# Kernel optimization log

Hardware: AMD Instinct MI355X
Metric: run time of the kernel (lower is better)

## Reference

```python
import jax, jax.numpy as jnp
import numpy as np

B, L, D = 4, 4096, 1024
NEG_BIG = -1e30  # finite stand-in for log(0) to keep vjp NaN-free; exp underflows to 0


def log_g(x):
    # log of g(x) = where(x>=0, x+0.5, sigmoid(x)); log-space, branch-safe
    return jnp.where(x >= 0.0, jnp.log(jax.nn.relu(x) + 0.5), -jax.nn.softplus(-x))


def setup_inputs() -> dict:
    key = jax.random.key(0)
    ks = jax.random.split(key, 4)
    std = np.sqrt(2.0 / D)  # kaiming_normal for fan_in = D
    x = jax.random.normal(ks[0], (B, L, D), dtype=jnp.float32)
    W_f = jax.random.normal(ks[1], (D, D), dtype=jnp.float32) * std
    W_i = jax.random.normal(ks[2], (D, D), dtype=jnp.float32) * std
    W_h = jax.random.normal(ks[3], (D, D), dtype=jnp.float32) * std
    b_f = jnp.zeros((D,), dtype=jnp.float32)
    b_i = jnp.zeros((D,), dtype=jnp.float32)
    b_h = jnp.zeros((D,), dtype=jnp.float32)
    return {"x": x, "W_f": W_f, "b_f": b_f, "W_i": W_i, "b_i": b_i, "W_h": W_h, "b_h": b_h}


def reference(x, W_f, b_f, W_i, b_i, W_h, b_h):
    # gate pre-activations: (B, L, D)
    f_pre = jnp.einsum('bld,ed->ble', x, W_f) + b_f
    i_pre = jnp.einsum('bld,ed->ble', x, W_i) + b_i
    h_pre = jnp.einsum('bld,ed->ble', x, W_h) + b_h

    # log-space normalized gates: log_f + log_i parametrize f/(f+i), i/(f+i)
    diff = jax.nn.softplus(-f_pre) - jax.nn.softplus(-i_pre)
    log_f = -jax.nn.softplus(diff)
    log_i = -jax.nn.softplus(-diff)
    log_tilde_h = log_g(h_pre)

    b, l, d = x.shape
    log_h0 = jnp.full((b, 1, d), NEG_BIG, dtype=x.dtype)  # log(0)
    log_values = jnp.concatenate([log_h0, log_i + log_tilde_h], axis=1)  # (B, L+1, D)

    # associative parallel scan in log space
    a_star = jnp.pad(jnp.cumsum(log_f, axis=1), ((0, 0), (1, 0), (0, 0)))  # (B, L+1, D)
    log_h = a_star + jax.lax.cumlogsumexp(log_values - a_star, axis=1)
    return jnp.exp(log_h)[:, 1:]  # (B, L, D)
```

## Files before the change

### kernel.cpp

```cpp
#include <hip/hip_runtime.h>

#define M_TOTAL 16384
#define N_DIM   1024
#define K_DIM   1024
#define L_SEQ   4096
#define B_SZ    4
#define D_DIM   1024
#define CH      64
#define NCHUNK  (L_SEQ / CH)
#define NCHAN   (B_SZ * D_DIM)

#define BM 128
#define BN 128
#define BK 64
#define NKT (K_DIM / BK)
#define TPB 512

typedef __attribute__((ext_vector_type(8))) short v8s;
typedef __attribute__((ext_vector_type(4))) float f32x4;

#define SB0()   __builtin_amdgcn_sched_barrier(0)
#define BAR()   __builtin_amdgcn_s_barrier()
#define WAITL0() do { asm volatile("s_waitcnt lgkmcnt(0)" ::: "memory"); SB0(); } while (0)
#define WAITL4() do { asm volatile("s_waitcnt lgkmcnt(4)" ::: "memory"); SB0(); } while (0)
#define WAITV0() do { asm volatile("s_waitcnt vmcnt(0)"   ::: "memory"); SB0(); } while (0)
#define AS1 __attribute__((address_space(1)))
#define AS3 __attribute__((address_space(3)))

__device__ __forceinline__ ushort f2b(float f) {
  uint u = __float_as_uint(f);
  u += 0x7FFFu + ((u >> 16) & 1u);
  return (ushort)(u >> 16);
}
__device__ __forceinline__ float b2f(ushort u) {
  return __uint_as_float(((uint)u) << 16);
}

__global__ void cast_f32_bf16(const float* __restrict__ src, ushort* __restrict__ dst, int n4) {
  int i = blockIdx.x * blockDim.x + threadIdx.x;
  if (i >= n4) return;
  float4 v = reinterpret_cast<const float4*>(src)[i];
  ushort4 o = make_ushort4(f2b(v.x), f2b(v.y), f2b(v.z), f2b(v.w));
  reinterpret_cast<ushort4*>(dst)[i] = o;
}

__device__ __forceinline__ void gates(float fp, float ip, float hp, float& a, float& v) {
  float Ef = __expf(-fp);
  float Ei = __expf(-ip);
  float r  = __builtin_amdgcn_rcpf(2.f + Ef + Ei);
  float f  = (1.f + Ei) * r;
  float i  = (1.f + Ef) * r;
  float ht = (hp >= 0.f) ? (hp + 0.5f) : __builtin_amdgcn_rcpf(1.f + __expf(-hp));
  a = f;
  v = i * ht;
}

__launch_bounds__(TPB, 2)
__global__ void gemm_fused(const ushort* __restrict__ X,
                           const ushort* __restrict__ W0, const ushort* __restrict__ W1,
                           const ushort* __restrict__ W2,
                           const float* __restrict__ bfp, const float* __restrict__ bip,
                           const float* __restrict__ bhp,
                           uint* __restrict__ Pav)
{
  __shared__ ushort lds[2][4][BM * BK];

  const int id = blockIdx.x;
  const int sw = (id & 7) * 128 + (id >> 3);
  const int n0 = (sw & 7) * BN;
  const int m0 = (sw >> 3) * BM;

  const int tid  = threadIdx.x;
  const int lane = tid & 63;
  const int w    = tid >> 6;
  const int wr   = w >> 2;
  const int wc   = w & 3;
  const int fr   = lane & 15, g = lane >> 4;

  int aoffh[4][2], boffh[2][2];
#pragma unroll
  for (int q = 0; q < 4; ++q)
#pragma unroll
    for (int ks = 0; ks < 2; ++ks) {
      int row = wr * 64 + q * 16 + fr;
      aoffh[q][ks] = row * BK + (((ks * 4 + g) ^ (row & 7)) << 3);
    }
#pragma unroll
  for (int n = 0; n < 2; ++n)
#pragma unroll
    for (int ks = 0; ks < 2; ++ks) {
      int row = wc * 32 + n * 16 + fr;
      boffh[n][ks] = row * BK + (((ks * 4 + g) ^ (row & 7)) << 3);
    }

  const int s0 = tid, s1 = 512 + tid;
  const int r0 = s0 >> 3, k0 = (s0 & 7) ^ (r0 & 7);
  const int r1 = s1 >> 3, k1 = (s1 & 7) ^ (r1 & 7);
  const int d0 = s0 * 8, d1 = s1 * 8;

  const ushort* gsrc[4][2];
  gsrc[0][0] = X  + (size_t)(m0 + r0) * K_DIM + k0 * 8;
  gsrc[0][1] = X  + (size_t)(m0 + r1) * K_DIM + k1 * 8;
  gsrc[1][0] = W0 + (size_t)(n0 + r0) * K_DIM + k0 * 8;
  gsrc[1][1] = W0 + (size_t)(n0 + r1) * K_DIM + k1 * 8;
  gsrc[2][0] = W1 + (size_t)(n0 + r0) * K_DIM + k0 * 8;
  gsrc[2][1] = W1 + (size_t)(n0 + r1) * K_DIM + k1 * 8;
  gsrc[3][0] = W2 + (size_t)(n0 + r0) * K_DIM + k0 * 8;
  gsrc[3][1] = W2 + (size_t)(n0 + r1) * K_DIM + k1 * 8;

  auto issue = [&](int buf, int mat, int kt, int j) {
    const ushort* s_ = gsrc[mat][j] + kt * BK;
    __builtin_amdgcn_global_load_lds((const AS1 void*)s_,
        (AS3 void*)(&lds[buf][mat][j ? d1 : d0]), 16, 0, 0);
  };

  f32x4 acc[3][4][2] = {};

#pragma unroll
  for (int mat = 0; mat < 4; ++mat) { issue(0, mat, 0, 0); issue(0, mat, 0, 1); }
  WAITV0();
  BAR(); SB0();

  int cur = 0;
  for (int t = 0; t < NKT; ++t) {
    const bool pf = (t + 1 < NKT);
    const ushort* rb = &lds[cur][0][0];
    v8s aF[4][2], bA[2][2], bB[2][2];

#pragma unroll
    for (int q = 0; q < 4; ++q)
#pragma unroll
      for (int ks = 0; ks < 2; ++ks)
        aF[q][ks] = *reinterpret_cast<const v8s*>(rb + aoffh[q][ks]);
#pragma unroll
    for (int n = 0; n < 2; ++n)
#pragma unroll
      for (int ks = 0; ks < 2; ++ks)
        bA[n][ks] = *reinterpret_cast<const v8s*>(rb + 1 * BM * BK + boffh[n][ks]);
    SB0();
    if (pf) {
#pragma unroll
      for (int mat = 0; mat < 4; ++mat) { issue(cur ^ 1, mat, t + 1, 0); issue(cur ^ 1, mat, t + 1, 1); }
    }
    SB0();
#pragma unroll
    for (int n = 0; n < 2; ++n)
#pragma unroll
      for (int ks = 0; ks < 2; ++ks)
        bB[n][ks] = *reinterpret_cast<const v8s*>(rb + 2 * BM * BK + boffh[n][ks]);
    SB0();
    WAITL4();
    __builtin_amdgcn_s_setprio(1);
#pragma unroll
    for (int ks = 0; ks < 2; ++ks)
#pragma unroll
      for (int mi = 0; mi < 4; ++mi) {
        acc[0][mi][0] = __builtin_amdgcn_mfma_f32_16x16x32_bf16(aF[mi][ks], bA[0][ks], acc[0][mi][0], 0, 0, 0);
        acc[0][mi][1] = __builtin_amdgcn_mfma_f32_16x16x32_bf16(aF[mi][ks], bA[1][ks], acc[0][mi][1], 0, 0, 0);
      }
    __builtin_amdgcn_s_setprio(0);
#pragma unroll
    for (int n = 0; n < 2; ++n)
#pragma unroll
      for (int ks = 0; ks < 2; ++ks)
        bA[n][ks] = *reinterpret_cast<const v8s*>(rb + 3 * BM * BK + boffh[n][ks]);
    SB0();
    WAITL4();
    __builtin_amdgcn_s_setprio(1);
#pragma unroll
    for (int ks = 0; ks < 2; ++ks)
#pragma unroll
      for (int mi = 0; mi < 4; ++mi) {
        acc[1][mi][0] = __builtin_amdgcn_mfma_f32_16x16x32_bf16(aF[mi][ks], bB[0][ks], acc[1][mi][0], 0, 0, 0);
        acc[1][mi][1] = __builtin_amdgcn_mfma_f32_16x16x32_bf16(aF[mi][ks], bB[1][ks], acc[1][mi][1], 0, 0, 0);
      }
    __builtin_amdgcn_s_setprio(0);
    WAITL0();
    __builtin_amdgcn_s_setprio(1);
#pragma unroll
    for (int ks = 0; ks < 2; ++ks)
#pragma unroll
      for (int mi = 0; mi < 4; ++mi) {
        acc[2][mi][0] = __builtin_amdgcn_mfma_f32_16x16x32_bf16(aF[mi][ks], bA[0][ks], acc[2][mi][0], 0, 0, 0);
        acc[2][mi][1] = __builtin_amdgcn_mfma_f32_16x16x32_bf16(aF[mi][ks], bA[1][ks], acc[2][mi][1], 0, 0, 0);
      }
    __builtin_amdgcn_s_setprio(0);

    if (pf) {
      WAITV0();
      BAR(); SB0();
      cur ^= 1;
    }
  }

#pragma unroll
  for (int ni = 0; ni < 2; ++ni) {
    const int col = n0 + wc * 32 + ni * 16 + fr;
    const float vbf = bfp[col], vbi = bip[col], vbh = bhp[col];
#pragma unroll
    for (int mi = 0; mi < 4; ++mi) {
      const int row0 = m0 + wr * 64 + mi * 16 + g * 4;
#pragma unroll
      for (int r = 0; r < 4; ++r) {
        float a, v;
        gates(acc[0][mi][ni][r] + vbf, acc[1][mi][ni][r] + vbi, acc[2][mi][ni][r] + vbh, a, v);
        Pav[(size_t)(row0 + r) * N_DIM + col] = (uint)f2b(a) | ((uint)f2b(v) << 16);
      }
    }
  }
}

__global__ void scan_pass1(const uint* __restrict__ Pav,
                           float* __restrict__ AggA, float* __restrict__ AggV)
{
  int tid = blockIdx.x * blockDim.x + threadIdx.x;
  int c = tid & (NCHAN - 1);
  int chunk = tid >> 12;
  int d = c & (D_DIM - 1);
  int b = c >> 10;
  size_t base = ((size_t)b * L_SEQ + (size_t)chunk * CH) * D_DIM + d;
  float A = 1.f, V = 0.f;
#pragma unroll 4
  for (int t = 0; t < CH; ++t) {
    uint u = Pav[base + (size_t)t * D_DIM];
    float a = b2f((ushort)(u & 0xFFFFu));
    float v = b2f((ushort)(u >> 16));
    A *= a;
    V = fmaf(a, V, v);
  }
  AggA[chunk * NCHAN + c] = A;
  AggV[chunk * NCHAN + c] = V;
}

__global__ void scan_mid(const float* __restrict__ AggA, const float* __restrict__ AggV,
                         float* __restrict__ Start)
{
  int c = blockIdx.x * blockDim.x + threadIdx.x;
  float h = 0.f;
#pragma unroll
  for (int j = 0; j < NCHUNK; ++j) {
    Start[j * NCHAN + c] = h;
    h = fmaf(AggA[j * NCHAN + c], h, AggV[j * NCHAN + c]);
  }
}

__global__ void scan_pass2(const uint* __restrict__ Pav,
                           const float* __restrict__ Start, float* __restrict__ out)
{
  int tid = blockIdx.x * blockDim.x + threadIdx.x;
  int c = tid & (NCHAN - 1);
  int chunk = tid >> 12;
  int d = c & (D_DIM - 1);
  int b = c >> 10;
  size_t base = ((size_t)b * L_SEQ + (size_t)chunk * CH) * D_DIM + d;
  float h = Start[chunk * NCHAN + c];
#pragma unroll 4
  for (int t = 0; t < CH; ++t) {
    size_t idx = base + (size_t)t * D_DIM;
    uint u = Pav[idx];
    float a = b2f((ushort)(u & 0xFFFFu));
    float v = b2f((ushort)(u >> 16));
    h = fmaf(a, h, v);
    out[idx] = h;
  }
}

extern "C" void kernel_launch(void* const* d_in, const int* in_sizes, int n_in,
                              void* d_out, int out_size, void* d_ws, size_t ws_size,
                              hipStream_t stream) {
  (void)in_sizes; (void)n_in; (void)out_size; (void)ws_size;
  const float* x  = (const float*)d_in[0];
  const float* Wf = (const float*)d_in[1];
  const float* bf = (const float*)d_in[2];
  const float* Wi = (const float*)d_in[3];
  const float* bi = (const float*)d_in[4];
  const float* Wh = (const float*)d_in[5];
  const float* bh = (const float*)d_in[6];
  float* out = (float*)d_out;

  ushort* xb  = (ushort*)d_ws;
  ushort* wfb = xb  + (size_t)M_TOTAL * K_DIM;
  ushort* wib = wfb + (size_t)N_DIM * K_DIM;
  ushort* whb = wib + (size_t)N_DIM * K_DIM;
  uint*  Pav  = (uint*)(whb + (size_t)N_DIM * K_DIM);
  float* AggA  = (float*)(Pav + (size_t)M_TOTAL * N_DIM);
  float* AggV  = AggA + NCHAN * NCHUNK;
  float* Start = AggV + NCHAN * NCHUNK;

  cast_f32_bf16<<<(M_TOTAL * K_DIM / 4) / 256, 256, 0, stream>>>(x,  xb,  M_TOTAL * K_DIM / 4);
  cast_f32_bf16<<<(N_DIM  * K_DIM / 4) / 256, 256, 0, stream>>>(Wf, wfb, N_DIM * K_DIM / 4);
  cast_f32_bf16<<<(N_DIM  * K_DIM / 4) / 256, 256, 0, stream>>>(Wi, wib, N_DIM * K_DIM / 4);
  cast_f32_bf16<<<(N_DIM  * K_DIM / 4) / 256, 256, 0, stream>>>(Wh, whb, N_DIM * K_DIM / 4);

  gemm_fused<<<dim3((M_TOTAL / BM) * (N_DIM / BN)), TPB, 0, stream>>>(
      xb, wfb, wib, whb, bf, bi, bh, Pav);

  scan_pass1<<<(NCHAN * NCHUNK) / 256, 256, 0, stream>>>(Pav, AggA, AggV);
  scan_mid<<<NCHAN / 256, 256, 0, stream>>>(AggA, AggV, Start);
  scan_pass2<<<(NCHAN * NCHUNK) / 256, 256, 0, stream>>>(Pav, Start, out);
}
```

Measured before the change: 189.8 us.

## Vectorize scan kernels to float4, merge weight casts, regroup GEMM tile order

The scan passes now process four channels per thread with 128-bit loads and stores, which cuts instruction count and raises bytes per memory request. The three weight casts are merged into one launch indexed by blockIdx.y. The GEMM block-to-tile mapping is regrouped so that each XCD's blocks cover 8x8 tile squares, for better L2 reuse. In exchange, the scan passes launch a quarter as many threads and scan_mid has less parallelism.

```diff
diff --git a/kernel.cpp b/kernel.cpp
--- a/kernel.cpp
+++ b/kernel.cpp
@@ -44,6 +44,17 @@
   reinterpret_cast<ushort4*>(dst)[i] = o;
 }
 
+__global__ void cast_w3(const float* __restrict__ s0, const float* __restrict__ s1,
+                        const float* __restrict__ s2,
+                        ushort* __restrict__ o0, ushort* __restrict__ o1, ushort* __restrict__ o2) {
+  int i = blockIdx.x * blockDim.x + threadIdx.x;
+  const float* s = (blockIdx.y == 0) ? s0 : (blockIdx.y == 1) ? s1 : s2;
+  ushort* o      = (blockIdx.y == 0) ? o0 : (blockIdx.y == 1) ? o1 : o2;
+  float4 v = reinterpret_cast<const float4*>(s)[i];
+  ushort4 t = make_ushort4(f2b(v.x), f2b(v.y), f2b(v.z), f2b(v.w));
+  reinterpret_cast<ushort4*>(o)[i] = t;
+}
+
 __device__ __forceinline__ void gates(float fp, float ip, float hp, float& a, float& v) {
   float Ef = __expf(-fp);
   float Ei = __expf(-ip);
@@ -65,10 +76,13 @@
 {
   __shared__ ushort lds[2][4][BM * BK];
 
-  const int id = blockIdx.x;
-  const int sw = (id & 7) * 128 + (id >> 3);
-  const int n0 = (sw & 7) * BN;
-  const int m0 = (sw >> 3) * BM;
+  const int id  = blockIdx.x;
+  const int x_  = id & 7;
+  const int k_  = id >> 3;
+  const int sub = k_ >> 6;
+  const int l2_ = k_ & 63;
+  const int n0 = (l2_ & 7) * BN;
+  const int m0 = (x_ * 16 + sub * 8 + (l2_ >> 3)) * BM;
 
   const int tid  = threadIdx.x;
   const int lane = tid & 63;
@@ -210,58 +224,69 @@
   }
 }
 
-__global__ void scan_pass1(const uint* __restrict__ Pav,
-                           float* __restrict__ AggA, float* __restrict__ AggV)
+__global__ void scan_pass1(const uint4* __restrict__ Pav4,
+                           float4* __restrict__ AggA, float4* __restrict__ AggV)
 {
   int tid = blockIdx.x * blockDim.x + threadIdx.x;
-  int c = tid & (NCHAN - 1);
-  int chunk = tid >> 12;
-  int d = c & (D_DIM - 1);
-  int b = c >> 10;
-  size_t base = ((size_t)b * L_SEQ + (size_t)chunk * CH) * D_DIM + d;
-  float A = 1.f, V = 0.f;
+  int c4 = tid & 1023;
+  int chunk = tid >> 10;
+  int b = c4 >> 8;
+  int d4 = c4 & 255;
+  size_t base4 = ((size_t)b * L_SEQ + (size_t)chunk * CH) * (D_DIM / 4) + d4;
+  float A0 = 1.f, A1 = 1.f, A2 = 1.f, A3 = 1.f;
+  float V0 = 0.f, V1 = 0.f, V2 = 0.f, V3 = 0.f;
 #pragma unroll 4
   for (int t = 0; t < CH; ++t) {
-    uint u = Pav[base + (size_t)t * D_DIM];
-    float a = b2f((ushort)(u & 0xFFFFu));
-    float v = b2f((ushort)(u >> 16));
-    A *= a;
-    V = fmaf(a, V, v);
-  }
-  AggA[chunk * NCHAN + c] = A;
-  AggV[chunk * NCHAN + c] = V;
-}
-
-__global__ void scan_mid(const float* __restrict__ AggA, const float* __restrict__ AggV,
-                         float* __restrict__ Start)
+    uint4 u = Pav4[base4 + (size_t)t * (D_DIM / 4)];
+    float a0 = b2f((ushort)(u.x & 0xFFFFu)), v0 = b2f((ushort)(u.x >> 16));
+    float a1 = b2f((ushort)(u.y & 0xFFFFu)), v1 = b2f((ushort)(u.y >> 16));
+    float a2 = b2f((ushort)(u.z & 0xFFFFu)), v2 = b2f((ushort)(u.z >> 16));
+    float a3 = b2f((ushort)(u.w & 0xFFFFu)), v3 = b2f((ushort)(u.w >> 16));
+    A0 *= a0; V0 = fmaf(a0, V0, v0);
+    A1 *= a1; V1 = fmaf(a1, V1, v1);
+    A2 *= a2; V2 = fmaf(a2, V2, v2);
+    A3 *= a3; V3 = fmaf(a3, V3, v3);
+  }
+  AggA[(size_t)chunk * (NCHAN / 4) + c4] = make_float4(A0, A1, A2, A3);
+  AggV[(size_t)chunk * (NCHAN / 4) + c4] = make_float4(V0, V1, V2, V3);
+}
+
+__global__ void scan_mid(const float4* __restrict__ AggA, const float4* __restrict__ AggV,
+                         float4* __restrict__ Start)
 {
-  int c = blockIdx.x * blockDim.x + threadIdx.x;
-  float h = 0.f;
+  int c4 = blockIdx.x * blockDim.x + threadIdx.x;
+  float4 h = make_float4(0.f, 0.f, 0.f, 0.f);
 #pragma unroll
   for (int j = 0; j < NCHUNK; ++j) {
-    Start[j * NCHAN + c] = h;
-    h = fmaf(AggA[j * NCHAN + c], h, AggV[j * NCHAN + c]);
-  }
-}
-
-__global__ void scan_pass2(const uint* __restrict__ Pav,
-                           const float* __restrict__ Start, float* __restrict__ out)
+    float4 A = AggA[(size_t)j * (NCHAN / 4) + c4];
+    float4 V = AggV[(size_t)j * (NCHAN / 4) + c4];
+    Start[(size_t)j * (NCHAN / 4) + c4] = h;
+    h.x = fmaf(A.x, h.x, V.x);
+    h.y = fmaf(A.y, h.y, V.y);
+    h.z = fmaf(A.z, h.z, V.z);
+    h.w = fmaf(A.w, h.w, V.w);
+  }
+}
+
+__global__ void scan_pass2(const uint4* __restrict__ Pav4,
+                           const float4* __restrict__ Start, float4* __restrict__ out4)
 {
   int tid = blockIdx.x * blockDim.x + threadIdx.x;
-  int c = tid & (NCHAN - 1);
-  int chunk = tid >> 12;
-  int d = c & (D_DIM - 1);
-  int b = c >> 10;
-  size_t base = ((size_t)b * L_SEQ + (size_t)chunk * CH) * D_DIM + d;
-  float h = Start[chunk * NCHAN + c];
+  int c4 = tid & 1023;
+  int chunk = tid >> 10;
+  int b = c4 >> 8;
+  int d4 = c4 & 255;
+  size_t base4 = ((size_t)b * L_SEQ + (size_t)chunk * CH) * (D_DIM / 4) + d4;
+  float4 h = Start[(size_t)chunk * (NCHAN / 4) + c4];
 #pragma unroll 4
   for (int t = 0; t < CH; ++t) {
-    size_t idx = base + (size_t)t * D_DIM;
-    uint u = Pav[idx];
-    float a = b2f((ushort)(u & 0xFFFFu));
-    float v = b2f((ushort)(u >> 16));
-    h = fmaf(a, h, v);
-    out[idx] = h;
+    size_t idx = base4 + (size_t)t * (D_DIM / 4);
+    uint4 u = Pav4[idx];
+    h.x = fmaf(b2f((ushort)(u.x & 0xFFFFu)), h.x, b2f((ushort)(u.x >> 16)));
+    h.y = fmaf(b2f((ushort)(u.y & 0xFFFFu)), h.y, b2f((ushort)(u.y >> 16)));
+    h.z = fmaf(b2f((ushort)(u.z & 0xFFFFu)), h.z, b2f((ushort)(u.z >> 16)));
+    h.w = fmaf(b2f((ushort)(u.w & 0xFFFFu)), h.w, b2f((ushort)(u.w >> 16)));
+    out4[idx] = h;
   }
 }
 
@@ -276,7 +301,6 @@
   const float* bi = (const float*)d_in[4];
   const float* Wh = (const float*)d_in[5];
   const float* bh = (const float*)d_in[6];
-  float* out = (float*)d_out;
 
   ushort* xb  = (ushort*)d_ws;
   ushort* wfb = xb  + (size_t)M_TOTAL * K_DIM;
@@ -287,15 +311,16 @@
   float* AggV  = AggA + NCHAN * NCHUNK;
   float* Start = AggV + NCHAN * NCHUNK;
 
-  cast_f32_bf16<<<(M_TOTAL * K_DIM / 4) / 256, 256, 0, stream>>>(x,  xb,  M_TOTAL * K_DIM / 4);
-  cast_f32_bf16<<<(N_DIM  * K_DIM / 4) / 256, 256, 0, stream>>>(Wf, wfb, N_DIM * K_DIM / 4);
-  cast_f32_bf16<<<(N_DIM  * K_DIM / 4) / 256, 256, 0, stream>>>(Wi, wib, N_DIM * K_DIM / 4);
-  cast_f32_bf16<<<(N_DIM  * K_DIM / 4) / 256, 256, 0, stream>>>(Wh, whb, N_DIM * K_DIM / 4);
+  cast_f32_bf16<<<(M_TOTAL * K_DIM / 4) / 256, 256, 0, stream>>>(x, xb, M_TOTAL * K_DIM / 4);
+  cast_w3<<<dim3((N_DIM * K_DIM / 4) / 256, 3), 256, 0, stream>>>(Wf, Wi, Wh, wfb, wib, whb);
 
   gemm_fused<<<dim3((M_TOTAL / BM) * (N_DIM / BN)), TPB, 0, stream>>>(
       xb, wfb, wib, whb, bf, bi, bh, Pav);
 
-  scan_pass1<<<(NCHAN * NCHUNK) / 256, 256, 0, stream>>>(Pav, AggA, AggV);
-  scan_mid<<<NCHAN / 256, 256, 0, stream>>>(AggA, AggV, Start);
-  scan_pass2<<<(NCHAN * NCHUNK) / 256, 256, 0, stream>>>(Pav, Start, out);
-}
+  scan_pass1<<<(NCHAN / 4 * NCHUNK) / 256, 256, 0, stream>>>(
+      (const uint4*)Pav, (float4*)AggA, (float4*)AggV);
+  scan_mid<<<(NCHAN / 4) / 256, 256, 0, stream>>>(
+      (const float4*)AggA, (const float4*)AggV, (float4*)Start);
+  scan_pass2<<<(NCHAN / 4 * NCHUNK) / 256, 256, 0, stream>>>(
+      (const uint4*)Pav, (const float4*)Start, (float4*)d_out);
+}
```

Measured after the change: 176.4 us. 7.1% less time.
